# Optimization experiments

Measured on AMD Instinct MI355X. Metric: run time of the kernel, lower is better.

## Reference

```python
import jax, jax.numpy as jnp
import numpy as np

B, S, R, Z, NLHS = 1024, 277, 76, 56, 24  # batch, seq_len, n_rules, z_size, n_lhs_symbols


def setup_inputs() -> dict:
    key = jax.random.key(0)
    k1, k2, k3, k4, k5, k6 = jax.random.split(key, 6)
    model_out_x = jax.random.normal(k1, (B, S, R), jnp.float32)
    mu = jax.random.normal(k2, (B, Z), jnp.float32)
    log_var = 0.1 * jax.random.normal(k3, (B, Z), jnp.float32)
    # one-hot targets over rules
    tgt_idx = jax.random.randint(k4, (B, S), 0, R)
    target_x = jax.nn.one_hot(tgt_idx, R, dtype=jnp.float32)
    # binary allowed-transition masks per LHS symbol
    masks = (jax.random.uniform(k5, (NLHS, R)) < 0.3).astype(jnp.float32)
    masks = masks.at[:, 0].set(1.0)  # ensure no all-zero mask row
    ind_to_lhs_ind = jax.random.randint(k6, (R,), 0, NLHS)
    return dict(model_out_x=model_out_x, mu=mu, log_var=log_var,
                target_x=target_x, masks=masks, ind_to_lhs_ind=ind_to_lhs_ind)


def reference(model_out_x, mu, log_var, target_x, masks, ind_to_lhs_ind):
    b = model_out_x.shape[0]
    seq_len = model_out_x.shape[1]
    z_size = mu.shape[1]

    # --- apply_masks: vectorized gather replacing the nested python loops ---
    true_rule = jnp.argmax(target_x, axis=-1)          # [B,S]
    lhs = ind_to_lhs_ind[true_rule]                    # [B,S]
    mask = masks[lhs]                                  # [B,S,R]
    shift_to_tiny = -100.0 + (model_out_x.min() - model_out_x.max())
    x = model_out_x + (1.0 - mask) * shift_to_tiny

    # --- softmax + BCE (torch BCELoss clamps log terms at -100) ---
    p = jax.nn.softmax(x, axis=-1)
    log_p = jnp.maximum(jnp.log(p), -100.0)
    log_1mp = jnp.maximum(jnp.log1p(-p), -100.0)
    bce = -jnp.mean(target_x * log_p + (1.0 - target_x) * log_1mp)
    BCE = seq_len * bce

    # --- moment-matching error on mu ---
    avg_mu = jnp.sum(mu, axis=0) / b                   # [Z]
    var = (mu.T @ mu) / b                              # [Z,Z]
    var_err = var - jnp.eye(z_size, dtype=mu.dtype)
    var_err = jnp.tanh(var_err) * var_err
    mom_err = jnp.sum(avg_mu * avg_mu) / z_size + jnp.sum(var_err) / (z_size * z_size)

    # sample_z=False, module in training mode -> loss = BCE + mom_err
    return BCE + mom_err
```

## Files before the change

### kernel.cpp

```cpp
#include <hip/hip_runtime.h>
#include <math.h>

#define BB    1024
#define SS    277
#define RR    76
#define ZZ    56
#define NLHS  24
#define NROWS (BB*SS)
#define ROWS_PER_BLOCK 64
#define NBCE (NROWS/ROWS_PER_BLOCK)
#define NMOM ZZ
#define NBLK (NBCE + NMOM)
#define V4_PER_BLOCK (ROWS_PER_BLOCK*RR/4)
#define BLK_ELEMS (ROWS_PER_BLOCK*RR)
#define TOTAL_ELEMS 21558272.0

static_assert(NROWS % ROWS_PER_BLOCK == 0, "rows divide blocks");

#define LN2F  0.69314718056f
#define NLN2F (-144.26950409f)

__global__ __launch_bounds__(64, 4) void fused_kernel(
    const float* __restrict__ model,
    const float* __restrict__ target,
    const float* __restrict__ masks,
    const int*   __restrict__ ind_to_lhs,
    const float* __restrict__ mu,
    double* __restrict__ partials)
{
    __shared__ unsigned int  smb[NLHS*4];
    __shared__ int           sm_lhs[RR];
    __shared__ unsigned char sm_idx[ROWS_PER_BLOCK];

    const int tid = threadIdx.x;

    if (blockIdx.x < NMOM) {
        const int j = blockIdx.x;
        const int i = (tid < ZZ) ? tid : 0;
        float dot = 0.f, s1 = 0.f;
        #pragma unroll 8
        for (int b = 0; b < BB; ++b) {
            const float c = mu[b*ZZ + j];
            const float a = mu[b*ZZ + i];
            dot = fmaf(a, c, dot);
            s1 += c;
        }
        float term = 0.f;
        if (tid < ZZ) {
            const float var = dot * (1.f/BB);
            const float ve  = var - ((tid == j) ? 1.f : 0.f);
            term = tanhf(ve) * ve * (1.f/(ZZ*ZZ));
            if (tid == j) {
                const float am = s1 * (1.f/BB);
                term = fmaf(am*am, 1.f/ZZ, term);
            }
        }
        #pragma unroll
        for (int off = 32; off; off >>= 1) term += __shfl_xor(term, off, 64);
        if (tid == 0) partials[blockIdx.x] = (double)term;
        return;
    }

    const int bce_blk = blockIdx.x - NMOM;

    if (tid < NLHS*4) smb[tid] = 0u;
    if (tid < NLHS*4 - 64) smb[64 + tid] = 0u;
    sm_idx[tid] = 0;
    __syncthreads();

    for (int e = tid; e < NLHS*RR; e += 64) {
        const int lhs = e / RR;
        const int r   = e - lhs*RR;
        if (masks[e] > 0.5f)
            atomicOr(&smb[lhs*4 + (r >> 5)], 1u << (r & 31));
    }
    for (int i = tid; i < RR; i += 64) sm_lhs[i] = ind_to_lhs[i];

    const size_t blk_base = (size_t)bce_blk * BLK_ELEMS;

    {
        const float4* t4 = (const float4*)(target + blk_base);
        #pragma unroll
        for (int k = 0; k < 19; ++k) {
            const int v4 = tid + 64*k;
            const float4 t = t4[v4];
            int he = -1;
            const int e = v4*4;
            if (t.x > 0.5f) he = e;
            if (t.y > 0.5f) he = e+1;
            if (t.z > 0.5f) he = e+2;
            if (t.w > 0.5f) he = e+3;
            if (he >= 0) {
                const int row = he / RR;
                sm_idx[row] = (unsigned char)(he - row*RR);
            }
        }
    }
    __syncthreads();

    const int true_r = (int)sm_idx[tid];
    const int lhs    = sm_lhs[true_r];
    const unsigned int mw0 = smb[lhs*4 + 0];
    const unsigned int mw1 = smb[lhs*4 + 1];
    const unsigned int mw2 = smb[lhs*4 + 2];

    const float4* m4 = (const float4*)(model + blk_base + (size_t)tid * RR);
    float4 x[19];
    #pragma unroll
    for (int k = 0; k < 19; ++k) x[k] = m4[k];

    float mx = -1e30f;
    #pragma unroll
    for (int k = 0; k < 19; ++k) {
        #pragma unroll
        for (int c = 0; c < 4; ++c) {
            const int r = k*4 + c;
            const unsigned int mw = (r < 32) ? mw0 : ((r < 64) ? mw1 : mw2);
            float* xp = (&x[k].x) + c;
            const bool un = (mw >> (r & 31)) & 1u;
            const float xm = un ? *xp : -1e30f;
            *xp = xm;
            mx = fmaxf(mx, xm);
        }
    }

    float s = 0.f;
    #pragma unroll
    for (int k = 0; k < 19; ++k) {
        #pragma unroll
        for (int c = 0; c < 4; ++c) {
            float* xp = (&x[k].x) + c;
            const float e = __expf(*xp - mx);
            *xp = e;
            s += e;
        }
    }

    const float inv = 1.f / s;
    float sum_l2 = 0.f;
    float p_true = 0.f;
    #pragma unroll
    for (int k = 0; k < 19; ++k) {
        #pragma unroll
        for (int c = 0; c < 4; ++c) {
            const int r = k*4 + c;
            const float p  = (&x[k].x)[c] * inv;
            const float l2 = __log2f(1.f - p);
            sum_l2 += fmaxf(l2, NLN2F);
            if (r == true_r) p_true = p;
        }
    }
    float row_sum = LN2F * sum_l2;
    const float l1c_t = fmaxf(LN2F * __log2f(1.f - p_true), -100.f);
    const float lp_t  = fmaxf(__logf(p_true), -100.f);
    row_sum += lp_t - l1c_t;

    #pragma unroll
    for (int off = 32; off; off >>= 1) row_sum += __shfl_xor(row_sum, off, 64);
    if (tid == 0) partials[blockIdx.x] = (double)row_sum;
}

__global__ __launch_bounds__(256) void final_kernel(
    const double* __restrict__ partials, float* __restrict__ out)
{
    __shared__ double sred[4];
    const int tid = threadIdx.x;
    double s = 0.0;
    for (int k = NMOM + tid; k < NBLK; k += 256) s += partials[k];
    double m = (tid < NMOM) ? partials[tid] : 0.0;
    double val = s * (-(double)SS / TOTAL_ELEMS) + m;
    #pragma unroll
    for (int off = 32; off; off >>= 1) val += __shfl_xor(val, off, 64);
    if ((tid & 63) == 0) sred[tid >> 6] = val;
    __syncthreads();
    if (tid == 0) out[0] = (float)((sred[0] + sred[1]) + (sred[2] + sred[3]));
}

extern "C" void kernel_launch(void* const* d_in, const int* in_sizes, int n_in,
                              void* d_out, int out_size, void* d_ws, size_t ws_size,
                              hipStream_t stream) {
    const float* model  = (const float*)d_in[0];
    const float* mu     = (const float*)d_in[1];
    const float* target = (const float*)d_in[3];
    const float* masks  = (const float*)d_in[4];
    const int*   ind    = (const int*)  d_in[5];
    float* out  = (float*)d_out;
    double* acc = (double*)d_ws;

    fused_kernel<<<NBLK, ROWS_PER_BLOCK, 0, stream>>>(model, target, masks, ind, mu, acc);
    final_kernel<<<1, 256, 0, stream>>>(acc, out);
}
```

Measured before the change: 239.2 us.

## Use 256-thread blocks and issue model loads before target scan

Grows BCE blocks from 64 to 256 rows, so each block does its mask-bitmap and lhs-table setup once per 256 rows rather than per 64. The model-row loads are now issued before the target one-hot scan and barrier, with empty asm pinning them so they overlap the scan's latency. The mu moment blocks split the batch loop across four waves and reduce through shared memory. This costs more registers held across the barrier and an extra block-level reduction.

```diff
diff --git a/kernel.cpp b/kernel.cpp
--- a/kernel.cpp
+++ b/kernel.cpp
@@ -7,7 +7,7 @@
 #define ZZ    56
 #define NLHS  24
 #define NROWS (BB*SS)
-#define ROWS_PER_BLOCK 64
+#define ROWS_PER_BLOCK 256
 #define NBCE (NROWS/ROWS_PER_BLOCK)
 #define NMOM ZZ
 #define NBLK (NBCE + NMOM)
@@ -20,7 +20,12 @@
 #define LN2F  0.69314718056f
 #define NLN2F (-144.26950409f)
 
-__global__ __launch_bounds__(64, 4) void fused_kernel(
+__device__ __forceinline__ float keep(float v) {
+    asm volatile("" : "+v"(v));
+    return v;
+}
+
+__global__ __launch_bounds__(256, 4) void fused_kernel(
     const float* __restrict__ model,
     const float* __restrict__ target,
     const float* __restrict__ masks,
@@ -31,58 +36,73 @@
     __shared__ unsigned int  smb[NLHS*4];
     __shared__ int           sm_lhs[RR];
     __shared__ unsigned char sm_idx[ROWS_PER_BLOCK];
+    __shared__ float         sm_red[4];
+    __shared__ float         sdot[4][64];
+    __shared__ float         ssum[4];
 
     const int tid = threadIdx.x;
 
     if (blockIdx.x < NMOM) {
-        const int j = blockIdx.x;
-        const int i = (tid < ZZ) ? tid : 0;
+        const int j    = blockIdx.x;
+        const int w    = tid >> 6;
+        const int lane = tid & 63;
+        const int i    = (lane < ZZ) ? lane : 0;
         float dot = 0.f, s1 = 0.f;
-        #pragma unroll 8
-        for (int b = 0; b < BB; ++b) {
+        const int b0 = 256*w;
+        #pragma unroll 4
+        for (int b = b0; b < b0 + 256; ++b) {
             const float c = mu[b*ZZ + j];
             const float a = mu[b*ZZ + i];
             dot = fmaf(a, c, dot);
             s1 += c;
         }
-        float term = 0.f;
-        if (tid < ZZ) {
-            const float var = dot * (1.f/BB);
-            const float ve  = var - ((tid == j) ? 1.f : 0.f);
-            term = tanhf(ve) * ve * (1.f/(ZZ*ZZ));
-            if (tid == j) {
-                const float am = s1 * (1.f/BB);
-                term = fmaf(am*am, 1.f/ZZ, term);
+        sdot[w][lane] = dot;
+        if (lane == 0) ssum[w] = s1;
+        __syncthreads();
+        if (w == 0) {
+            float term = 0.f;
+            if (lane < ZZ) {
+                const float var = (sdot[0][lane]+sdot[1][lane]+sdot[2][lane]+sdot[3][lane]) * (1.f/BB);
+                const float ve  = var - ((lane == j) ? 1.f : 0.f);
+                term = tanhf(ve) * ve * (1.f/(ZZ*ZZ));
+                if (lane == j) {
+                    const float am = (ssum[0]+ssum[1]+ssum[2]+ssum[3]) * (1.f/BB);
+                    term = fmaf(am*am, 1.f/ZZ, term);
+                }
             }
-        }
-        #pragma unroll
-        for (int off = 32; off; off >>= 1) term += __shfl_xor(term, off, 64);
-        if (tid == 0) partials[blockIdx.x] = (double)term;
+            #pragma unroll
+            for (int off = 32; off; off >>= 1) term += __shfl_xor(term, off, 64);
+            if (lane == 0) partials[blockIdx.x] = (double)term;
+        }
         return;
     }
 
     const int bce_blk = blockIdx.x - NMOM;
 
     if (tid < NLHS*4) smb[tid] = 0u;
-    if (tid < NLHS*4 - 64) smb[64 + tid] = 0u;
     sm_idx[tid] = 0;
     __syncthreads();
 
-    for (int e = tid; e < NLHS*RR; e += 64) {
+    for (int e = tid; e < NLHS*RR; e += 256) {
         const int lhs = e / RR;
         const int r   = e - lhs*RR;
         if (masks[e] > 0.5f)
             atomicOr(&smb[lhs*4 + (r >> 5)], 1u << (r & 31));
     }
-    for (int i = tid; i < RR; i += 64) sm_lhs[i] = ind_to_lhs[i];
+    if (tid < RR) sm_lhs[tid] = ind_to_lhs[tid];
 
     const size_t blk_base = (size_t)bce_blk * BLK_ELEMS;
+
+    const float4* m4 = (const float4*)(model + blk_base + (size_t)tid * RR);
+    float4 x[19];
+    #pragma unroll
+    for (int k = 0; k < 19; ++k) x[k] = m4[k];
 
     {
         const float4* t4 = (const float4*)(target + blk_base);
         #pragma unroll
         for (int k = 0; k < 19; ++k) {
-            const int v4 = tid + 64*k;
+            const int v4 = tid + 256*k;
             const float4 t = t4[v4];
             int he = -1;
             const int e = v4*4;
@@ -98,16 +118,17 @@
     }
     __syncthreads();
 
+    #pragma unroll
+    for (int k = 0; k < 19; ++k) {
+        x[k].x = keep(x[k].x); x[k].y = keep(x[k].y);
+        x[k].z = keep(x[k].z); x[k].w = keep(x[k].w);
+    }
+
     const int true_r = (int)sm_idx[tid];
     const int lhs    = sm_lhs[true_r];
     const unsigned int mw0 = smb[lhs*4 + 0];
     const unsigned int mw1 = smb[lhs*4 + 1];
     const unsigned int mw2 = smb[lhs*4 + 2];
-
-    const float4* m4 = (const float4*)(model + blk_base + (size_t)tid * RR);
-    float4 x[19];
-    #pragma unroll
-    for (int k = 0; k < 19; ++k) x[k] = m4[k];
 
     float mx = -1e30f;
     #pragma unroll
@@ -157,7 +178,10 @@
 
     #pragma unroll
     for (int off = 32; off; off >>= 1) row_sum += __shfl_xor(row_sum, off, 64);
-    if (tid == 0) partials[blockIdx.x] = (double)row_sum;
+    if ((tid & 63) == 0) sm_red[tid >> 6] = row_sum;
+    __syncthreads();
+    if (tid == 0)
+        partials[blockIdx.x] = (double)((sm_red[0] + sm_red[1]) + (sm_red[2] + sm_red[3]));
 }
 
 __global__ __launch_bounds__(256) void final_kernel(
```

Measured after the change: 215.6 us. -9.9%, faster.
